# Kernel tuning notes

Measured on AMD Instinct MI355X. Metric: run time of the kernel, lower is better.

Reference implementation:

```python
import jax, jax.numpy as jnp
import numpy as np

B, L, D, H = 4, 1024, 1024, 16
HD = D // H
SCALE = 1.0 / np.sqrt(HD)
NOISE_PROB = 0.05
NOISE_SCALE = 0.1


def _linear(x, w, b):
    # torch nn.Linear convention: y = x @ W^T + b, W: [out, in]
    return x @ w.T + b


def _quantum_noise(key, real, imag, p=NOISE_PROB, s=NOISE_SCALE):
    """Phase flips, amplitude noise, and measurement dropout on a complex
    tensor represented as (real, imag). Deterministic given `key`."""
    k_phase, k_amp, k_nr, k_ni, k_meas = jax.random.split(key, 5)
    shape = real.shape
    flip = jnp.where(jax.random.uniform(k_phase, shape) < p, -1.0, 1.0)
    amp_mask = (jax.random.uniform(k_amp, shape) < p).astype(real.dtype)
    new_r = real * flip + jax.random.normal(k_nr, shape, real.dtype) * s * amp_mask
    new_i = imag * flip + jax.random.normal(k_ni, shape, imag.dtype) * s * amp_mask
    keep = 1.0 - (jax.random.uniform(k_meas, shape) < p * 0.5).astype(real.dtype)
    return new_r * keep, new_i * keep


def _heads(t):
    # [B, L, D] -> [B, H, L, HD]
    b, l, _ = t.shape
    return t.reshape(b, l, H, HD).transpose(0, 2, 1, 3)


def setup_inputs() -> dict:
    key = jax.random.key(0)
    ks = jax.random.split(key, 16)
    inp = {
        "x_real": jax.random.normal(ks[0], (B, L, D), jnp.float32),
        "x_imag": jax.random.normal(ks[1], (B, L, D), jnp.float32),
        "mask": jnp.ones((B, L), jnp.int32),
    }
    names = ["qr", "qi", "kr", "ki", "vr", "vi", "or", "oi"]
    for i, n in enumerate(names):
        inp[n + "_w"] = jax.random.normal(ks[2 + i], (D, D), jnp.float32) * 0.02
        inp[n + "_b"] = jnp.zeros((D,), jnp.float32)
    ent = jnp.eye(H) + (jax.random.normal(ks[10], (H, H)) * 0.1) * (
        jax.random.uniform(ks[11], (H, H)) < 0.2
    ).astype(jnp.float32)
    inp["ent"] = ent
    return inp


def reference(x_real, x_imag, mask, qr_w, qr_b, qi_w, qi_b, kr_w, kr_b,
              ki_w, ki_b, vr_w, vr_b, vi_w, vi_b, or_w, or_b, oi_w, oi_b, ent):
    # complex Q/K/V: real part from x.real, imag part from x.imag
    q_r, q_i = _linear(x_real, qr_w, qr_b), _linear(x_imag, qi_w, qi_b)
    k_r, k_i = _linear(x_real, kr_w, kr_b), _linear(x_imag, ki_w, ki_b)
    v_r, v_i = _linear(x_real, vr_w, vr_b), _linear(x_imag, vi_w, vi_b)

    nkey = jax.random.key(1)
    q_r, q_i = _quantum_noise(jax.random.fold_in(nkey, 0), q_r, q_i)
    k_r, k_i = _quantum_noise(jax.random.fold_in(nkey, 1), k_r, k_i)
    v_r, v_i = _quantum_noise(jax.random.fold_in(nkey, 2), v_r, v_i)

    q_r, q_i, k_r, k_i, v_r, v_i = map(_heads, (q_r, q_i, k_r, k_i, v_r, v_i))

    # torch.einsum('bhld,hh->bhld') == per-head scaling by diag(ent)
    d = jnp.diagonal(ent)[None, :, None, None]
    q_r, q_i = q_r * d, q_i * d
    k_r, k_i = k_r * d, k_i * d

    # Re(q . conj(k)) interference score: [B, H, Lq, Lk]
    scores = (jnp.einsum("bhqd,bhkd->bhqk", q_r, k_r)
              + jnp.einsum("bhqd,bhkd->bhqk", q_i, k_i)) * SCALE
    scores = jnp.where(mask[:, None, None, :] == 0, -1e9, scores)
    attn = jax.nn.softmax(scores, axis=-1)

    out_r = jnp.einsum("bhqk,bhkd->bhqd", attn, v_r)
    out_i = jnp.einsum("bhqk,bhkd->bhqd", attn, v_i)
    out_r = out_r.transpose(0, 2, 1, 3).reshape(x_real.shape)
    out_i = out_i.transpose(0, 2, 1, 3).reshape(x_real.shape)

    out_real = _linear(out_r, or_w, or_b)
    out_imag = _linear(out_i, oi_w, oi_b)
    return out_real, out_imag, attn
```

## Files before the change

kernel.cpp:

```cpp
#include <hip/hip_runtime.h>
#include <cstdint>

#define PARTITIONABLE 1

static constexpr int Bsz = 4, Lsz = 1024, Dsz = 1024, Hn = 16, HDsz = 64;
static constexpr size_t ELEMS = (size_t)Bsz * Lsz * Dsz;
static constexpr uint32_t HALF_N = (uint32_t)(ELEMS / 2);
static constexpr float SCALE = 0.125f;
static constexpr float P_NOISE = 0.05f;
static constexpr float S_NOISE = 0.1f;
static constexpr size_t MBy = 1024 * 1024;

typedef unsigned short u16;
typedef uint64_t u64;
typedef __attribute__((ext_vector_type(8))) short short8v;
typedef __attribute__((ext_vector_type(4))) float floatx4;
typedef __attribute__((ext_vector_type(4))) unsigned int uint4v;

__device__ __forceinline__ void gload16(const u16* g, u16* l) {
  __builtin_amdgcn_global_load_lds(
      (const __attribute__((address_space(1))) void*)(g),
      (__attribute__((address_space(3))) void*)(l), 16, 0, 0);
}

__host__ __device__ __forceinline__ void tf2x32(uint32_t k0, uint32_t k1,
                                                uint32_t x0, uint32_t x1,
                                                uint32_t& o0, uint32_t& o1) {
  uint32_t ks2 = k0 ^ k1 ^ 0x1BD11BDAu;
  x0 += k0; x1 += k1;
#define TFR(r) { x0 += x1; x1 = (x1 << (r)) | (x1 >> (32 - (r))); x1 ^= x0; }
  TFR(13) TFR(15) TFR(26) TFR(6)
  x0 += k1; x1 += ks2 + 1u;
  TFR(17) TFR(29) TFR(16) TFR(24)
  x0 += ks2; x1 += k0 + 2u;
  TFR(13) TFR(15) TFR(26) TFR(6)
  x0 += k0; x1 += k1 + 3u;
  TFR(17) TFR(29) TFR(16) TFR(24)
  x0 += k1; x1 += ks2 + 4u;
  TFR(13) TFR(15) TFR(26) TFR(6)
  x0 += ks2; x1 += k0 + 5u;
#undef TFR
  o0 = x0; o1 = x1;
}

struct KeySet { uint32_t k[5][2]; };
struct AllKeys { KeySet t[3]; };

__device__ __forceinline__ uint32_t draw_bits(uint32_t k0, uint32_t k1, uint32_t idx) {
#if PARTITIONABLE
  uint32_t o0, o1; tf2x32(k0, k1, 0u, idx, o0, o1);
  return o0 ^ o1;
#else
  uint32_t o0, o1;
  if (idx < HALF_N) { tf2x32(k0, k1, idx, idx + HALF_N, o0, o1); return o0; }
  tf2x32(k0, k1, idx - HALF_N, idx, o0, o1); return o1;
#endif
}

__device__ __forceinline__ float unif01(uint32_t bits) {
  return __uint_as_float((bits >> 9) | 0x3f800000u) - 1.0f;
}

__device__ __forceinline__ float normal_from_bits(uint32_t bits) {
  const float LO = -0.99999994f;
  float f = unif01(bits);
  float x = fmaxf(LO, f * 2.0f + LO);
  float w = -log1pf(-x * x);
  float p;
  if (w < 5.0f) {
    w = w - 2.5f;
    p = 2.81022636e-08f;
    p = fmaf(p, w, 3.43273939e-07f);
    p = fmaf(p, w, -3.5233877e-06f);
    p = fmaf(p, w, -4.39150654e-06f);
    p = fmaf(p, w, 0.00021858087f);
    p = fmaf(p, w, -0.00125372503f);
    p = fmaf(p, w, -0.00417768164f);
    p = fmaf(p, w, 0.246640727f);
    p = fmaf(p, w, 1.50140941f);
  } else {
    w = sqrtf(w) - 3.0f;
    p = -0.000200214257f;
    p = fmaf(p, w, 0.000100950558f);
    p = fmaf(p, w, 0.00134934322f);
    p = fmaf(p, w, -0.00367342844f);
    p = fmaf(p, w, 0.00573950773f);
    p = fmaf(p, w, -0.0076224613f);
    p = fmaf(p, w, 0.00943887047f);
    p = fmaf(p, w, 1.00167406f);
    p = fmaf(p, w, 2.83297682f);
  }
  return 1.41421356f * (p * x);
}

__device__ __forceinline__ uint32_t bf16_rn(float f) {
  uint32_t u = __float_as_uint(f);
  return (u + 0x7FFFu + ((u >> 16) & 1u)) >> 16;
}
__device__ __forceinline__ float bf2f(uint32_t h) { return __uint_as_float(h << 16); }
__device__ __forceinline__ void cvt_split(float4 v, u64& hi, u64& lo) {
  uint32_t h0 = bf16_rn(v.x), h1 = bf16_rn(v.y), h2 = bf16_rn(v.z), h3 = bf16_rn(v.w);
  float r0 = v.x - bf2f(h0), r1 = v.y - bf2f(h1), r2 = v.z - bf2f(h2), r3 = v.w - bf2f(h3);
  uint32_t l0 = bf16_rn(r0), l1 = bf16_rn(r1), l2 = bf16_rn(r2), l3 = bf16_rn(r3);
  hi = (u64)h0 | ((u64)h1 << 16) | ((u64)h2 << 32) | ((u64)h3 << 48);
  lo = (u64)l0 | ((u64)l1 << 16) | ((u64)l2 << 32) | ((u64)l3 << 48);
}

__device__ __forceinline__ void mfma_tile(const u16* Ahs, const u16* Als,
                                          const u16* Bhs, const u16* Bls,
                                          int l, int wm, int wn, floatx4 acc[4][4]) {
#pragma unroll
  for (int c = 0; c < 2; ++c) {
    const int pr = (l ^ (l >> 4) ^ (c << 2)) & 63;
    short8v aH[4], aL[4], bH[4], bL[4];
#pragma unroll
    for (int t = 0; t < 4; ++t) {
      const int ia = ((c * 8 + wm * 4 + t) * 64 + pr) * 8;
      aH[t] = *(const short8v*)&Ahs[ia]; aL[t] = *(const short8v*)&Als[ia];
      const int ib = ((c * 8 + wn * 4 + t) * 64 + pr) * 8;
      bH[t] = *(const short8v*)&Bhs[ib]; bL[t] = *(const short8v*)&Bls[ib];
    }
#pragma unroll
    for (int mt = 0; mt < 4; ++mt)
#pragma unroll
      for (int nt = 0; nt < 4; ++nt) {
        acc[mt][nt] = __builtin_amdgcn_mfma_f32_16x16x32_bf16(aH[mt], bH[nt], acc[mt][nt], 0, 0, 0);
        acc[mt][nt] = __builtin_amdgcn_mfma_f32_16x16x32_bf16(aH[mt], bL[nt], acc[mt][nt], 0, 0, 0);
        acc[mt][nt] = __builtin_amdgcn_mfma_f32_16x16x32_bf16(aL[mt], bH[nt], acc[mt][nt], 0, 0, 0);
      }
  }
}

__device__ __forceinline__ void mfma_step(const u16* Ahs, const u16* Als,
                                          const u16* Bhs, const u16* Bls,
                                          int pr, int wm, int wn, floatx4 acc[4][4]) {
  short8v aH[4], aL[4], bH[4], bL[4];
#pragma unroll
  for (int t = 0; t < 4; ++t) {
    const int ia = ((wm * 4 + t) * 64 + pr) * 8;
    aH[t] = *(const short8v*)&Ahs[ia]; aL[t] = *(const short8v*)&Als[ia];
    const int ib = ((wn * 4 + t) * 64 + pr) * 8;
    bH[t] = *(const short8v*)&Bhs[ib]; bL[t] = *(const short8v*)&Bls[ib];
  }
#pragma unroll
  for (int mt = 0; mt < 4; ++mt)
#pragma unroll
    for (int nt = 0; nt < 4; ++nt) {
      acc[mt][nt] = __builtin_amdgcn_mfma_f32_16x16x32_bf16(aH[mt], bH[nt], acc[mt][nt], 0, 0, 0);
      acc[mt][nt] = __builtin_amdgcn_mfma_f32_16x16x32_bf16(aH[mt], bL[nt], acc[mt][nt], 0, 0, 0);
      acc[mt][nt] = __builtin_amdgcn_mfma_f32_16x16x32_bf16(aL[mt], bH[nt], acc[mt][nt], 0, 0, 0);
    }
}

struct SJob { const float* src; u16* dh; u16* dl; int n4; };
struct SJobs { SJob j[8]; };

__global__ __launch_bounds__(256) void split8_kernel(SJobs js) {
  const SJob J = js.j[blockIdx.y];
  int i = blockIdx.x * 256 + (int)threadIdx.x;
  if (i >= J.n4) return;
  float4 v = ((const float4*)J.src)[i];
  u64 h, l; cvt_split(v, h, l);
  ((u64*)J.dh)[i] = h; ((u64*)J.dl)[i] = l;
}

struct GJob { const u16* Ah; const u16* Al; const u16* Wh; const u16* Wl;
              const float* bias; float* Yf; u16* Yh; u16* Yl; };
struct GJobs { GJob j[6]; };

template<int MODE>
__global__ __launch_bounds__(256, 2) void gemm_kernel(GJobs jobs) {
  const GJob J = jobs.j[blockIdx.z];
  const int n0 = blockIdx.x * 128, m0 = blockIdx.y * 128;
  __shared__ u16 Ahs[8192], Als[8192], Bhs[8192], Bls[8192];
  const int tid = (int)threadIdx.x, w = tid >> 6, l = tid & 63;
  const int wm = w >> 1, wn = w & 1;
  const int cA = w >> 1, m2A = l >> 4;
  const int qA = (l ^ m2A ^ (cA << 2)) & 15;
  const int colA = cA * 32 + m2A * 8;
  const int tb = (w & 1) * 4;

  const u16* ahp = J.Ah + (size_t)(m0 + qA) * Dsz + colA;
  const u16* alp = J.Al + (size_t)(m0 + qA) * Dsz + colA;
  const u16* whp = J.Wh + (size_t)(n0 + qA) * Dsz + colA;
  const u16* wlp = J.Wl + (size_t)(n0 + qA) * Dsz + colA;

  floatx4 acc[4][4];
#pragma unroll
  for (int i = 0; i < 4; ++i)
#pragma unroll
    for (int j = 0; j < 4; ++j) acc[i][j] = (floatx4){0.f, 0.f, 0.f, 0.f};

  for (int k0 = 0; k0 < Dsz; k0 += 64) {
    __syncthreads();
#pragma unroll
    for (int i = 0; i < 4; ++i) {
      const size_t go = (size_t)((tb + i) * 16) * Dsz + k0;
      gload16(ahp + go, &Ahs[(w * 4 + i) * 512]);
      gload16(alp + go, &Als[(w * 4 + i) * 512]);
      gload16(whp + go, &Bhs[(w * 4 + i) * 512]);
      gload16(wlp + go, &Bls[(w * 4 + i) * 512]);
    }
    __syncthreads();
    mfma_tile(Ahs, Als, Bhs, Bls, l, wm, wn, acc);
  }

  const int colLane = l & 15, rquad = l >> 4;
#pragma unroll
  for (int nt = 0; nt < 4; ++nt) {
    const int col = n0 + wn * 64 + nt * 16 + colLane;
    const float bv = J.bias[col];
#pragma unroll
    for (int mt = 0; mt < 4; ++mt) {
      const int r0 = m0 + wm * 64 + mt * 16 + rquad * 4;
#pragma unroll
      for (int j2 = 0; j2 < 4; ++j2) {
        float v = acc[mt][nt][j2] + bv;
        if (MODE == 1) {
          J.Yf[(size_t)(r0 + j2) * Dsz + col] = v;
        } else {
          const uint32_t hi = bf16_rn(v);
          const uint32_t lo = bf16_rn(v - bf2f(hi));
          J.Yh[(size_t)(r0 + j2) * Dsz + col] = (u16)hi;
          J.Yl[(size_t)(r0 + j2) * Dsz + col] = (u16)lo;
        }
      }
    }
  }
}

__global__ __launch_bounds__(256) void noise_kernel(
    u16* __restrict__ qhr, u16* __restrict__ qlr, u16* __restrict__ qhi, u16* __restrict__ qli,
    u16* __restrict__ khr, u16* __restrict__ klr, u16* __restrict__ khi, u16* __restrict__ kli,
    u16* __restrict__ vhr, u16* __restrict__ vlr, u16* __restrict__ vhi, u16* __restrict__ vli,
    const float* __restrict__ ent, AllKeys keys) {
  const uint32_t e = blockIdx.x * 256u + threadIdx.x;
  const int j = (int)blockIdx.y;
  u16 *rh, *rl, *ih, *il;
  if (j == 0) { rh = qhr; rl = qlr; ih = qhi; il = qli; }
  else if (j == 1) { rh = khr; rl = klr; ih = khi; il = kli; }
  else { rh = vhr; rl = vlr; ih = vhi; il = vli; }
  const KeySet& ks = keys.t[j];
  const uint32_t b_phase = draw_bits(ks.k[0][0], ks.k[0][1], e);
  const uint32_t b_amp   = draw_bits(ks.k[1][0], ks.k[1][1], e);
  const uint32_t b_nr    = draw_bits(ks.k[2][0], ks.k[2][1], e);
  const uint32_t b_ni    = draw_bits(ks.k[3][0], ks.k[3][1], e);
  const uint32_t b_meas  = draw_bits(ks.k[4][0], ks.k[4][1], e);
  const float flip = (unif01(b_phase) < P_NOISE) ? -1.0f : 1.0f;
  const float amp  = (unif01(b_amp)  < P_NOISE) ? 1.0f : 0.0f;
  const float keep = (unif01(b_meas) < P_NOISE * 0.5f) ? 0.0f : 1.0f;
  const float nr = normal_from_bits(b_nr);
  const float ni = normal_from_bits(b_ni);
  float r  = bf2f(rh[e]) + bf2f(rl[e]);
  float iv = bf2f(ih[e]) + bf2f(il[e]);
  r  = (r  * flip + nr * S_NOISE * amp) * keep;
  iv = (iv * flip + ni * S_NOISE * amp) * keep;
  if (j != 2) {
    const int h = ((int)e & (Dsz - 1)) >> 6;
    const float d = ent[h * Hn + h];
    r *= d; iv *= d;
  }
  uint32_t hr = bf16_rn(r);  rh[e] = (u16)hr; rl[e] = (u16)bf16_rn(r - bf2f(hr));
  uint32_t hi2 = bf16_rn(iv); ih[e] = (u16)hi2; il[e] = (u16)bf16_rn(iv - bf2f(hi2));
}

__global__ __launch_bounds__(256, 2) void scores_kernel(
    const u16* __restrict__ qhr, const u16* __restrict__ qlr,
    const u16* __restrict__ qhi, const u16* __restrict__ qli,
    const u16* __restrict__ khr, const u16* __restrict__ klr,
    const u16* __restrict__ khi, const u16* __restrict__ kli,
    const int* __restrict__ mask, float* __restrict__ attn) {
  const int bh = (int)blockIdx.z;
  const int b = bh >> 4, h = bh & 15;
  const int n0 = blockIdx.x * 128, m0 = blockIdx.y * 128;
  __shared__ u16 Ahs[2][4096], Als[2][4096], Bhs[2][4096], Bls[2][4096];
  const int tid = (int)threadIdx.x, w = tid >> 6, l = tid & 63;
  const int wm = w >> 1, wn = w & 1;
  const int qA = (l ^ (l >> 4)) & 15, colA = (l >> 4) * 8;
  const int pr = (l ^ (l >> 4)) & 63;
  const int t0 = w * 2, t1 = w * 2 + 1;

  const size_t aoff = ((size_t)(b * Lsz) + m0 + qA) * Dsz + h * HDsz + colA;
  const size_t boff = ((size_t)(b * Lsz) + n0 + qA) * Dsz + h * HDsz + colA;

  floatx4 acc[4][4];
#pragma unroll
  for (int i = 0; i < 4; ++i)
#pragma unroll
    for (int j = 0; j < 4; ++j) acc[i][j] = (floatx4){0.f, 0.f, 0.f, 0.f};

#define STGS(bufi, AH, AL, BH, BL, K0V) { \
    const size_t g0 = (size_t)(t0 * 16) * Dsz + (K0V); \
    const size_t g1 = (size_t)(t1 * 16) * Dsz + (K0V); \
    gload16(AH + aoff + g0, &Ahs[bufi][t0 * 512]); gload16(AH + aoff + g1, &Ahs[bufi][t1 * 512]); \
    gload16(AL + aoff + g0, &Als[bufi][t0 * 512]); gload16(AL + aoff + g1, &Als[bufi][t1 * 512]); \
    gload16(BH + boff + g0, &Bhs[bufi][t0 * 512]); gload16(BH + boff + g1, &Bhs[bufi][t1 * 512]); \
    gload16(BL + boff + g0, &Bls[bufi][t0 * 512]); gload16(BL + boff + g1, &Bls[bufi][t1 * 512]); }

  STGS(0, qhr, qlr, khr, klr, 0)
  __syncthreads();
  STGS(1, qhr, qlr, khr, klr, 32)
  mfma_step(Ahs[0], Als[0], Bhs[0], Bls[0], pr, wm, wn, acc);
  __syncthreads();
  STGS(0, qhi, qli, khi, kli, 0)
  mfma_step(Ahs[1], Als[1], Bhs[1], Bls[1], pr, wm, wn, acc);
  __syncthreads();
  STGS(1, qhi, qli, khi, kli, 32)
  mfma_step(Ahs[0], Als[0], Bhs[0], Bls[0], pr, wm, wn, acc);
  __syncthreads();
  mfma_step(Ahs[1], Als[1], Bhs[1], Bls[1], pr, wm, wn, acc);
#undef STGS

  const int colLane = l & 15, rquad = l >> 4;
#pragma unroll
  for (int nt = 0; nt < 4; ++nt) {
    const int col = n0 + wn * 64 + nt * 16 + colLane;
    const int mv = mask[b * Lsz + col];
#pragma unroll
    for (int mt = 0; mt < 4; ++mt) {
      const int r0 = m0 + wm * 64 + mt * 16 + rquad * 4;
#pragma unroll
      for (int j = 0; j < 4; ++j)
        attn[((size_t)bh * Lsz + r0 + j) * Lsz + col] =
            (mv == 0) ? -1e9f : acc[mt][nt][j] * SCALE;
    }
  }
}

__global__ __launch_bounds__(256) void vtrans_kernel(
    const u16* __restrict__ vhr, const u16* __restrict__ vlr,
    const u16* __restrict__ vhi, const u16* __restrict__ vli,
    u16* __restrict__ vth, u16* __restrict__ vtl) {
  const int bh = (int)blockIdx.y;
  const int b = bh >> 4, h = bh & 15;
  const int k0 = blockIdx.x * 64;
  __shared__ uint32_t T[128 * 65];
  const int t = (int)threadIdx.x;
  const int krow = t >> 4, d4 = (t & 15) * 4;

#pragma unroll
  for (int src = 0; src < 2; ++src) {
    const u16* VH = src ? vhi : vhr;
    const u16* VL = src ? vli : vlr;
    const int nb = src * 64;
#pragma unroll
    for (int p = 0; p < 4; ++p) {
      const int k = p * 16 + krow;
      const size_t off = ((size_t)(b * Lsz) + k0 + k) * Dsz + h * HDsz + d4;
      u64 hv = *(const u64*)(VH + off);
      u64 lv = *(const u64*)(VL + off);
#pragma unroll
      for (int e = 0; e < 4; ++e) {
        uint32_t hi = (uint32_t)((hv >> (16 * e)) & 0xFFFFu);
        uint32_t lo = (uint32_t)((lv >> (16 * e)) & 0xFFFFu);
        T[(nb + d4 + e) * 65 + k] = lo | (hi << 16);
      }
    }
  }
  __syncthreads();
  const int n = t >> 1, hf = t & 1;
  const size_t rowb = ((size_t)bh * 128 + n) * Lsz + k0 + hf * 32;
#pragma unroll
  for (int g = 0; g < 4; ++g) {
    uint32_t wv[8];
#pragma unroll
    for (int u = 0; u < 8; ++u) wv[u] = T[n * 65 + hf * 32 + g * 8 + u];
    uint4v hvv, lvv;
    hvv.x = (wv[0] >> 16) | (wv[1] & 0xFFFF0000u);
    hvv.y = (wv[2] >> 16) | (wv[3] & 0xFFFF0000u);
    hvv.z = (wv[4] >> 16) | (wv[5] & 0xFFFF0000u);
    hvv.w = (wv[6] >> 16) | (wv[7] & 0xFFFF0000u);
    lvv.x = (wv[0] & 0xFFFFu) | (wv[1] << 16);
    lvv.y = (wv[2] & 0xFFFFu) | (wv[3] << 16);
    lvv.z = (wv[4] & 0xFFFFu) | (wv[5] << 16);
    lvv.w = (wv[6] & 0xFFFFu) | (wv[7] << 16);
    *(uint4v*)&vth[rowb + g * 8] = hvv;
    *(uint4v*)&vtl[rowb + g * 8] = lvv;
  }
}

__global__ __launch_bounds__(256) void rowstat_kernel(const float* __restrict__ S,
                                                      float* __restrict__ rowm,
                                                      float* __restrict__ rowsum) {
  const int wv = (int)threadIdx.x >> 6, lane = (int)threadIdx.x & 63;
  const size_t row = (size_t)blockIdx.x * 4 + wv;
  const float* p = S + row * Lsz;
  float4 v[4];
#pragma unroll
  for (int i = 0; i < 4; ++i) v[i] = *(const float4*)(p + i * 256 + lane * 4);
  float m = -3.402823466e38f;
#pragma unroll
  for (int i = 0; i < 4; ++i)
    m = fmaxf(m, fmaxf(fmaxf(v[i].x, v[i].y), fmaxf(v[i].z, v[i].w)));
#pragma unroll
  for (int d = 1; d < 64; d <<= 1) m = fmaxf(m, __shfl_xor(m, d));
  float s = 0.f;
#pragma unroll
  for (int i = 0; i < 4; ++i)
    s += expf(v[i].x - m) + expf(v[i].y - m) + expf(v[i].z - m) + expf(v[i].w - m);
#pragma unroll
  for (int d = 1; d < 64; d <<= 1) s += __shfl_xor(s, d);
  if (lane == 0) { rowm[row] = m; rowsum[row] = s; }
}

__global__ __launch_bounds__(256, 2) void pv_kernel(
    float* __restrict__ attn, const u16* __restrict__ vth, const u16* __restrict__ vtl,
    const float* __restrict__ rowm, const float* __restrict__ rowsum,
    u16* __restrict__ ohr, u16* __restrict__ olr,
    u16* __restrict__ ohi, u16* __restrict__ oli) {
  const int bh = (int)blockIdx.y;
  const int b = bh >> 4, h = bh & 15;
  const int m0 = blockIdx.x * 128;
  __shared__ u16 Ahs[2][4096], Als[2][4096], Bhs[2][4096], Bls[2][4096];
  const int tid = (int)threadIdx.x, w = tid >> 6, l = tid & 63;
  const int wm = w >> 1, wn = w & 1;
  const int qA = (l ^ (l >> 4)) & 15, colA = (l >> 4) * 8;
  const int pr = (l ^ (l >> 4)) & 63;
  const int t0 = w * 2, t1 = w * 2 + 1;

  const int ar = tid >> 3, akq = tid & 7;
  const int am2 = akq >> 1, ahalf = akq & 1;
  int aidx[4];
  float rmv[4], inv[4];
#pragma unroll
  for (int rr = 0; rr < 4; ++rr) {
    const int trow = ar + rr * 32;
    const int p = ((trow & 15) + 16 * am2) ^ am2;
    aidx[rr] = ((trow >> 4) * 64 + p) * 8 + ahalf * 4;
    const size_t grow = (size_t)bh * Lsz + m0 + trow;
    rmv[rr] = rowm[grow]; inv[rr] = 1.0f / rowsum[grow];
  }
  float* arp = attn + ((size_t)bh * Lsz + m0 + ar) * Lsz + akq * 4;
  const u16* bhp = vth + ((size_t)bh * 128 + qA) * Lsz + colA;
  const u16* blp = vtl + ((size_t)bh * 128 + qA) * Lsz + colA;

  floatx4 acc[4][4];
#pragma unroll
  for (int i = 0; i < 4; ++i)
#pragma unroll
    for (int j = 0; j < 4; ++j) acc[i][j] = (floatx4){0.f, 0.f, 0.f, 0.f};

#define STGB(bufi, K0V) { \
    const size_t g0 = (size_t)(t0 * 16) * Lsz + (K0V); \
    const size_t g1 = (size_t)(t1 * 16) * Lsz + (K0V); \
    gload16(bhp + g0, &Bhs[bufi][t0 * 512]); gload16(bhp + g1, &Bhs[bufi][t1 * 512]); \
    gload16(blp + g0, &Bls[bufi][t0 * 512]); gload16(blp + g1, &Bls[bufi][t1 * 512]); }

#define LOADA(K0V, A4) { \
    _Pragma("unroll") for (int rr = 0; rr < 4; ++rr) \
      A4[rr] = *(const float4*)(arp + (size_t)(rr * 32) * Lsz + (K0V)); }

#define PROCA(bufi, K0V, A4) { \
    _Pragma("unroll") for (int rr = 0; rr < 4; ++rr) { \
      float4 p4; \
      p4.x = expf(A4[rr].x - rmv[rr]) * inv[rr]; \
      p4.y = expf(A4[rr].y - rmv[rr]) * inv[rr]; \
      p4.z = expf(A4[rr].z - rmv[rr]) * inv[rr]; \
      p4.w = expf(A4[rr].w - rmv[rr]) * inv[rr]; \
      *(float4*)(arp + (size_t)(rr * 32) * Lsz + (K0V)) = p4; \
      u64 h64, l64; cvt_split(p4, h64, l64); \
      *(u64*)&Ahs[bufi][aidx[rr]] = h64; *(u64*)&Als[bufi][aidx[rr]] = l64; } }

  {
    float4 a4[4];
    LOADA(0, a4)
    STGB(0, 0)
    PROCA(0, 0, a4)
  }
  __syncthreads();
  for (int kt = 0; kt < 32; kt += 2) {
    float4 n4[4];
    if (kt + 1 < 32) { LOADA((size_t)(kt + 1) * 32, n4) STGB(1, (size_t)(kt + 1) * 32) }
    mfma_step(Ahs[0], Als[0], Bhs[0], Bls[0], pr, wm, wn, acc);
    if (kt + 1 < 32) PROCA(1, (size_t)(kt + 1) * 32, n4)
    __syncthreads();
    if (kt + 2 < 32) { LOADA((size_t)(kt + 2) * 32, n4) STGB(0, (size_t)(kt + 2) * 32) }
    mfma_step(Ahs[1], Als[1], Bhs[1], Bls[1], pr, wm, wn, acc);
    if (kt + 2 < 32) PROCA(0, (size_t)(kt + 2) * 32, n4)
    __syncthreads();
  }
#undef STGB
#undef LOADA
#undef PROCA

  const int colLane = l & 15, rquad = l >> 4;
#pragma unroll
  for (int nt = 0; nt < 4; ++nt) {
    const int col = wn * 64 + nt * 16 + colLane;
    u16* oh = (col < 64) ? ohr : ohi;
    u16* ol = (col < 64) ? olr : oli;
    const int dcol = col & 63;
#pragma unroll
    for (int mt = 0; mt < 4; ++mt) {
      const int r0 = m0 + wm * 64 + mt * 16 + rquad * 4;
#pragma unroll
      for (int j = 0; j < 4; ++j) {
        float v = acc[mt][nt][j];
        const uint32_t hi = bf16_rn(v);
        const uint32_t lo = bf16_rn(v - bf2f(hi));
        const size_t oidx = ((size_t)(b * Lsz) + r0 + j) * Dsz + h * HDsz + dcol;
        oh[oidx] = (u16)hi; ol[oidx] = (u16)lo;
      }
    }
  }
}

extern "C" void kernel_launch(void* const* d_in, const int* in_sizes, int n_in,
                              void* d_out, int out_size, void* d_ws, size_t ws_size,
                              hipStream_t stream) {
  const float* x_real = (const float*)d_in[0];
  const float* x_imag = (const float*)d_in[1];
  const int*   mask   = (const int*)d_in[2];
  const float* pw[6] = {(const float*)d_in[3], (const float*)d_in[5], (const float*)d_in[7],
                        (const float*)d_in[9], (const float*)d_in[11], (const float*)d_in[13]};
  const float* pb[6] = {(const float*)d_in[4], (const float*)d_in[6], (const float*)d_in[8],
                        (const float*)d_in[10], (const float*)d_in[12], (const float*)d_in[14]};
  const float* or_w = (const float*)d_in[15]; const float* or_b = (const float*)d_in[16];
  const float* oi_w = (const float*)d_in[17]; const float* oi_b = (const float*)d_in[18];
  const float* ent  = (const float*)d_in[19];

  float* out_real = (float*)d_out;
  float* out_imag = out_real + ELEMS;
  float* attn     = out_imag + ELEMS;

  if (ws_size < 96 * MBy) return;
  uint8_t* wsb = (uint8_t*)d_ws;
  u16* qhr = (u16*)(wsb + 0 * MBy);  u16* qlr = (u16*)(wsb + 8 * MBy);
  u16* qhi = (u16*)(wsb + 16 * MBy); u16* qli = (u16*)(wsb + 24 * MBy);
  u16* khr = (u16*)(wsb + 32 * MBy); u16* klr = (u16*)(wsb + 40 * MBy);
  u16* khi = (u16*)(wsb + 48 * MBy); u16* kli = (u16*)(wsb + 56 * MBy);
  u16* xhr = (u16*)(wsb + 64 * MBy); u16* xlr = (u16*)(wsb + 72 * MBy);
  u16* xhi = (u16*)(wsb + 80 * MBy); u16* xli = (u16*)(wsb + 88 * MBy);
  u16* vth = (u16*)(wsb + 64 * MBy); u16* vtl = (u16*)(wsb + 80 * MBy);
  u16* ohr = (u16*)(wsb + 0 * MBy);  u16* olr = (u16*)(wsb + 8 * MBy);
  u16* ohi = (u16*)(wsb + 16 * MBy); u16* oli = (u16*)(wsb + 24 * MBy);
  u16* owh[2] = {(u16*)(wsb + 32 * MBy), (u16*)(wsb + 36 * MBy)};
  u16* owl[2] = {(u16*)(wsb + 34 * MBy), (u16*)(wsb + 38 * MBy)};

  uint8_t* atb = (uint8_t*)attn;
  u16* vhr = (u16*)(atb + 0 * MBy);  u16* vlr = (u16*)(atb + 8 * MBy);
  u16* vhi = (u16*)(atb + 16 * MBy); u16* vli = (u16*)(atb + 24 * MBy);

  float* rowm = out_real;
  float* rowsum = out_real + 65536;

  AllKeys keys;
  for (int j = 0; j < 3; ++j) {
    uint32_t a, b2;
    tf2x32(0u, 1u, 0u, (uint32_t)j, a, b2);
#if PARTITIONABLE
    for (int i = 0; i < 5; ++i)
      tf2x32(a, b2, 0u, (uint32_t)i, keys.t[j].k[i][0], keys.t[j].k[i][1]);
#else
    uint32_t out10[10];
    for (int i = 0; i < 5; ++i) {
      uint32_t o0, o1; tf2x32(a, b2, (uint32_t)i, (uint32_t)(i + 5), o0, o1);
      out10[i] = o0; out10[i + 5] = o1;
    }
    for (int i = 0; i < 5; ++i) { keys.t[j].k[i][0] = out10[2*i]; keys.t[j].k[i][1] = out10[2*i+1]; }
#endif
  }

  u16* pwh[6]; u16* pwl[6];
  for (int z = 0; z < 6; ++z) {
    pwh[z] = (u16*)(atb + 32 * MBy + (size_t)z * 4 * MBy);
    pwl[z] = pwh[z] + (size_t)Dsz * Dsz;
  }
  SJobs sj{};
  sj.j[0] = {x_real, xhr, xlr, (int)(ELEMS / 4)};
  sj.j[1] = {x_imag, xhi, xli, (int)(ELEMS / 4)};
  for (int z = 0; z < 6; ++z) sj.j[2 + z] = {pw[z], pwh[z], pwl[z], Dsz * Dsz / 4};
  split8_kernel<<<dim3(4096, 8), 256, 0, stream>>>(sj);

  GJobs pj{};
  u16* yh[6] = {qhr, qhi, khr, khi, vhr, vhi};
  u16* yl[6] = {qlr, qli, klr, kli, vlr, vli};
  const u16* ah6[6] = {xhr, xhi, xhr, xhi, xhr, xhi};
  const u16* al6[6] = {xlr, xli, xlr, xli, xlr, xli};
  for (int z = 0; z < 6; ++z) {
    pj.j[z].Ah = ah6[z]; pj.j[z].Al = al6[z];
    pj.j[z].Wh = pwh[z]; pj.j[z].Wl = pwl[z];
    pj.j[z].bias = pb[z]; pj.j[z].Yf = nullptr; pj.j[z].Yh = yh[z]; pj.j[z].Yl = yl[z];
  }
  gemm_kernel<0><<<dim3(8, 32, 6), 256, 0, stream>>>(pj);

  noise_kernel<<<dim3((uint32_t)(ELEMS / 256), 3), 256, 0, stream>>>(
      qhr, qlr, qhi, qli, khr, klr, khi, kli, vhr, vlr, vhi, vli, ent, keys);

  vtrans_kernel<<<dim3(16, 64), 256, 0, stream>>>(vhr, vlr, vhi, vli, vth, vtl);

  scores_kernel<<<dim3(8, 8, 64), 256, 0, stream>>>(
      qhr, qlr, qhi, qli, khr, klr, khi, kli, mask, attn);

  SJobs so{};
  so.j[0] = {or_w, owh[0], owl[0], Dsz * Dsz / 4};
  so.j[1] = {oi_w, owh[1], owl[1], Dsz * Dsz / 4};
  split8_kernel<<<dim3(1024, 2), 256, 0, stream>>>(so);

  rowstat_kernel<<<dim3(16384), 256, 0, stream>>>(attn, rowm, rowsum);

  pv_kernel<<<dim3(8, 64), 256, 0, stream>>>(attn, vth, vtl, rowm, rowsum,
                                             ohr, olr, ohi, oli);

  GJobs oj{};
  oj.j[0].Ah = ohr; oj.j[0].Al = olr; oj.j[0].Wh = owh[0]; oj.j[0].Wl = owl[0];
  oj.j[0].bias = or_b; oj.j[0].Yf = out_real;
  oj.j[1].Ah = ohi; oj.j[1].Al = oli; oj.j[1].Wh = owh[1]; oj.j[1].Wl = owl[1];
  oj.j[1].bias = oi_b; oj.j[1].Yf = out_imag;
  gemm_kernel<1><<<dim3(8, 32, 2), 256, 0, stream>>>(oj);
}
```

Measured before the change: 821.4 us.

## Fuse softmax row statistics into scores epilogue and double-buffer projection GEMM

The scores kernel now computes per-tile row max and sum-of-exponentials in its epilogue, reducing them across lanes and warps into per-block partials. A small rowstat2 kernel merges the 8 partials per row, replacing a pass that re-read the full 256MB score matrix. Separately, the projection GEMM is restructured to double-buffer LDS with 32-wide K steps so global-to-LDS loads overlap MFMA work. The cost is extra epilogue exp and shuffle work in the scores kernel plus a partials scratch buffer placed inside out_real.

```diff
diff --git a/kernel.cpp b/kernel.cpp
--- a/kernel.cpp
+++ b/kernel.cpp
@@ -106,31 +106,6 @@
   lo = (u64)l0 | ((u64)l1 << 16) | ((u64)l2 << 32) | ((u64)l3 << 48);
 }
 
-__device__ __forceinline__ void mfma_tile(const u16* Ahs, const u16* Als,
-                                          const u16* Bhs, const u16* Bls,
-                                          int l, int wm, int wn, floatx4 acc[4][4]) {
-#pragma unroll
-  for (int c = 0; c < 2; ++c) {
-    const int pr = (l ^ (l >> 4) ^ (c << 2)) & 63;
-    short8v aH[4], aL[4], bH[4], bL[4];
-#pragma unroll
-    for (int t = 0; t < 4; ++t) {
-      const int ia = ((c * 8 + wm * 4 + t) * 64 + pr) * 8;
-      aH[t] = *(const short8v*)&Ahs[ia]; aL[t] = *(const short8v*)&Als[ia];
-      const int ib = ((c * 8 + wn * 4 + t) * 64 + pr) * 8;
-      bH[t] = *(const short8v*)&Bhs[ib]; bL[t] = *(const short8v*)&Bls[ib];
-    }
-#pragma unroll
-    for (int mt = 0; mt < 4; ++mt)
-#pragma unroll
-      for (int nt = 0; nt < 4; ++nt) {
-        acc[mt][nt] = __builtin_amdgcn_mfma_f32_16x16x32_bf16(aH[mt], bH[nt], acc[mt][nt], 0, 0, 0);
-        acc[mt][nt] = __builtin_amdgcn_mfma_f32_16x16x32_bf16(aH[mt], bL[nt], acc[mt][nt], 0, 0, 0);
-        acc[mt][nt] = __builtin_amdgcn_mfma_f32_16x16x32_bf16(aL[mt], bH[nt], acc[mt][nt], 0, 0, 0);
-      }
-  }
-}
-
 __device__ __forceinline__ void mfma_step(const u16* Ahs, const u16* Als,
                                           const u16* Bhs, const u16* Bls,
                                           int pr, int wm, int wn, floatx4 acc[4][4]) {
@@ -172,13 +147,12 @@
 __global__ __launch_bounds__(256, 2) void gemm_kernel(GJobs jobs) {
   const GJob J = jobs.j[blockIdx.z];
   const int n0 = blockIdx.x * 128, m0 = blockIdx.y * 128;
-  __shared__ u16 Ahs[8192], Als[8192], Bhs[8192], Bls[8192];
+  __shared__ u16 Ahs[2][4096], Als[2][4096], Bhs[2][4096], Bls[2][4096];
   const int tid = (int)threadIdx.x, w = tid >> 6, l = tid & 63;
   const int wm = w >> 1, wn = w & 1;
-  const int cA = w >> 1, m2A = l >> 4;
-  const int qA = (l ^ m2A ^ (cA << 2)) & 15;
-  const int colA = cA * 32 + m2A * 8;
-  const int tb = (w & 1) * 4;
+  const int qA = (l ^ (l >> 4)) & 15, colA = (l >> 4) * 8;
+  const int pr = (l ^ (l >> 4)) & 63;
+  const int t0 = w * 2, t1 = w * 2 + 1;
 
   const u16* ahp = J.Ah + (size_t)(m0 + qA) * Dsz + colA;
   const u16* alp = J.Al + (size_t)(m0 + qA) * Dsz + colA;
@@ -191,19 +165,25 @@
 #pragma unroll
     for (int j = 0; j < 4; ++j) acc[i][j] = (floatx4){0.f, 0.f, 0.f, 0.f};
 
-  for (int k0 = 0; k0 < Dsz; k0 += 64) {
+#define STG(bufi, K0V) { \
+    const size_t g0 = (size_t)(t0 * 16) * Dsz + (K0V); \
+    const size_t g1 = (size_t)(t1 * 16) * Dsz + (K0V); \
+    gload16(ahp + g0, &Ahs[bufi][t0 * 512]); gload16(ahp + g1, &Ahs[bufi][t1 * 512]); \
+    gload16(alp + g0, &Als[bufi][t0 * 512]); gload16(alp + g1, &Als[bufi][t1 * 512]); \
+    gload16(whp + g0, &Bhs[bufi][t0 * 512]); gload16(whp + g1, &Bhs[bufi][t1 * 512]); \
+    gload16(wlp + g0, &Bls[bufi][t0 * 512]); gload16(wlp + g1, &Bls[bufi][t1 * 512]); }
+
+  STG(0, 0)
+  __syncthreads();
+  for (int kt = 0; kt < 32; kt += 2) {
+    if (kt + 1 < 32) STG(1, (size_t)(kt + 1) * 32)
+    mfma_step(Ahs[0], Als[0], Bhs[0], Bls[0], pr, wm, wn, acc);
     __syncthreads();
-#pragma unroll
-    for (int i = 0; i < 4; ++i) {
-      const size_t go = (size_t)((tb + i) * 16) * Dsz + k0;
-      gload16(ahp + go, &Ahs[(w * 4 + i) * 512]);
-      gload16(alp + go, &Als[(w * 4 + i) * 512]);
-      gload16(whp + go, &Bhs[(w * 4 + i) * 512]);
-      gload16(wlp + go, &Bls[(w * 4 + i) * 512]);
-    }
+    if (kt + 2 < 32) STG(0, (size_t)(kt + 2) * 32)
+    mfma_step(Ahs[1], Als[1], Bhs[1], Bls[1], pr, wm, wn, acc);
     __syncthreads();
-    mfma_tile(Ahs, Als, Bhs, Bls, l, wm, wn, acc);
-  }
+  }
+#undef STG
 
   const int colLane = l & 15, rquad = l >> 4;
 #pragma unroll
@@ -269,11 +249,13 @@
     const u16* __restrict__ qhi, const u16* __restrict__ qli,
     const u16* __restrict__ khr, const u16* __restrict__ klr,
     const u16* __restrict__ khi, const u16* __restrict__ kli,
-    const int* __restrict__ mask, float* __restrict__ attn) {
+    const int* __restrict__ mask, float* __restrict__ attn,
+    float2* __restrict__ part) {
   const int bh = (int)blockIdx.z;
   const int b = bh >> 4, h = bh & 15;
   const int n0 = blockIdx.x * 128, m0 = blockIdx.y * 128;
   __shared__ u16 Ahs[2][4096], Als[2][4096], Bhs[2][4096], Bls[2][4096];
+  __shared__ float2 pstat[2][128];
   const int tid = (int)threadIdx.x, w = tid >> 6, l = tid & 63;
   const int wm = w >> 1, wn = w & 1;
   const int qA = (l ^ (l >> 4)) & 15, colA = (l >> 4) * 8;
@@ -312,19 +294,73 @@
 #undef STGS
 
   const int colLane = l & 15, rquad = l >> 4;
-#pragma unroll
-  for (int nt = 0; nt < 4; ++nt) {
-    const int col = n0 + wn * 64 + nt * 16 + colLane;
-    const int mv = mask[b * Lsz + col];
-#pragma unroll
-    for (int mt = 0; mt < 4; ++mt) {
-      const int r0 = m0 + wm * 64 + mt * 16 + rquad * 4;
+  int mv4[4];
+#pragma unroll
+  for (int nt = 0; nt < 4; ++nt)
+    mv4[nt] = mask[b * Lsz + n0 + wn * 64 + nt * 16 + colLane];
+
+  float sm[4][4], ss[4][4];
+#pragma unroll
+  for (int mt = 0; mt < 4; ++mt) {
+    const int r0 = m0 + wm * 64 + mt * 16 + rquad * 4;
+#pragma unroll
+    for (int j = 0; j < 4; ++j) {
+      float v4[4];
+#pragma unroll
+      for (int nt = 0; nt < 4; ++nt) {
+        const int col = n0 + wn * 64 + nt * 16 + colLane;
+        float v = (mv4[nt] == 0) ? -1e9f : acc[mt][nt][j] * SCALE;
+        attn[((size_t)bh * Lsz + r0 + j) * Lsz + col] = v;
+        v4[nt] = v;
+      }
+      float m4 = fmaxf(fmaxf(v4[0], v4[1]), fmaxf(v4[2], v4[3]));
+      float s4 = expf(v4[0] - m4) + expf(v4[1] - m4) + expf(v4[2] - m4) + expf(v4[3] - m4);
+      sm[mt][j] = m4; ss[mt][j] = s4;
+    }
+  }
+#pragma unroll
+  for (int d = 1; d < 16; d <<= 1) {
+#pragma unroll
+    for (int mt = 0; mt < 4; ++mt)
+#pragma unroll
+      for (int j = 0; j < 4; ++j) {
+        float om = __shfl_xor(sm[mt][j], d);
+        float os = __shfl_xor(ss[mt][j], d);
+        float mn = fmaxf(sm[mt][j], om);
+        ss[mt][j] = ss[mt][j] * expf(sm[mt][j] - mn) + os * expf(om - mn);
+        sm[mt][j] = mn;
+      }
+  }
+  if (colLane == 0) {
+#pragma unroll
+    for (int mt = 0; mt < 4; ++mt)
 #pragma unroll
       for (int j = 0; j < 4; ++j)
-        attn[((size_t)bh * Lsz + r0 + j) * Lsz + col] =
-            (mv == 0) ? -1e9f : acc[mt][nt][j] * SCALE;
-    }
-  }
+        pstat[wn][wm * 64 + mt * 16 + rquad * 4 + j] = make_float2(sm[mt][j], ss[mt][j]);
+  }
+  __syncthreads();
+  if (tid < 128) {
+    float2 a = pstat[0][tid], c = pstat[1][tid];
+    float mn = fmaxf(a.x, c.x);
+    float s = a.y * expf(a.x - mn) + c.y * expf(c.x - mn);
+    part[((size_t)bh * Lsz + m0 + tid) * 8 + blockIdx.x] = make_float2(mn, s);
+  }
+}
+
+__global__ __launch_bounds__(256) void rowstat2_kernel(const float2* __restrict__ part,
+                                                       float* __restrict__ rowm,
+                                                       float* __restrict__ rowsum) {
+  const size_t row = (size_t)blockIdx.x * 256 + threadIdx.x;
+  float2 p[8];
+#pragma unroll
+  for (int i = 0; i < 8; ++i) p[i] = part[row * 8 + i];
+  float m = p[0].x;
+#pragma unroll
+  for (int i = 1; i < 8; ++i) m = fmaxf(m, p[i].x);
+  float s = 0.f;
+#pragma unroll
+  for (int i = 0; i < 8; ++i) s += p[i].y * expf(p[i].x - m);
+  rowm[row] = m; rowsum[row] = s;
 }
 
 __global__ __launch_bounds__(256) void vtrans_kernel(
@@ -377,30 +413,6 @@
     *(uint4v*)&vth[rowb + g * 8] = hvv;
     *(uint4v*)&vtl[rowb + g * 8] = lvv;
   }
-}
-
-__global__ __launch_bounds__(256) void rowstat_kernel(const float* __restrict__ S,
-                                                      float* __restrict__ rowm,
-                                                      float* __restrict__ rowsum) {
-  const int wv = (int)threadIdx.x >> 6, lane = (int)threadIdx.x & 63;
-  const size_t row = (size_t)blockIdx.x * 4 + wv;
-  const float* p = S + row * Lsz;
-  float4 v[4];
-#pragma unroll
-  for (int i = 0; i < 4; ++i) v[i] = *(const float4*)(p + i * 256 + lane * 4);
-  float m = -3.402823466e38f;
-#pragma unroll
-  for (int i = 0; i < 4; ++i)
-    m = fmaxf(m, fmaxf(fmaxf(v[i].x, v[i].y), fmaxf(v[i].z, v[i].w)));
-#pragma unroll
-  for (int d = 1; d < 64; d <<= 1) m = fmaxf(m, __shfl_xor(m, d));
-  float s = 0.f;
-#pragma unroll
-  for (int i = 0; i < 4; ++i)
-    s += expf(v[i].x - m) + expf(v[i].y - m) + expf(v[i].z - m) + expf(v[i].w - m);
-#pragma unroll
-  for (int d = 1; d < 64; d <<= 1) s += __shfl_xor(s, d);
-  if (lane == 0) { rowm[row] = m; rowsum[row] = s; }
 }
 
 __global__ __launch_bounds__(256, 2) void pv_kernel(
@@ -543,6 +555,7 @@
 
   float* rowm = out_real;
   float* rowsum = out_real + 65536;
+  float2* part = (float2*)(out_real + 131072);
 
   AllKeys keys;
   for (int j = 0; j < 3; ++j) {
@@ -590,14 +603,14 @@
   vtrans_kernel<<<dim3(16, 64), 256, 0, stream>>>(vhr, vlr, vhi, vli, vth, vtl);
 
   scores_kernel<<<dim3(8, 8, 64), 256, 0, stream>>>(
-      qhr, qlr, qhi, qli, khr, klr, khi, kli, mask, attn);
+      qhr, qlr, qhi, qli, khr, klr, khi, kli, mask, attn, part);
 
   SJobs so{};
   so.j[0] = {or_w, owh[0], owl[0], Dsz * Dsz / 4};
   so.j[1] = {oi_w, owh[1], owl[1], Dsz * Dsz / 4};
   split8_kernel<<<dim3(1024, 2), 256, 0, stream>>>(so);
 
-  rowstat_kernel<<<dim3(16384), 256, 0, stream>>>(attn, rowm, rowsum);
+  rowstat2_kernel<<<dim3(256), 256, 0, stream>>>(part, rowm, rowsum);
 
   pv_kernel<<<dim3(8, 64), 256, 0, stream>>>(attn, vth, vtl, rowm, rowsum,
                                              ohr, olr, ohi, oli);
```

Measured after the change: 854.9 us. 4.1% more time.

## Fuse Q/K/V projections sharing an input into one GEMM kernel

Applied to the files above, without the earlier changes.

The projection GEMM now computes Q, K and V for the same input (real or imag) in one block, loading each A tile once and reusing it across three weight matrices. K-step drops from 64 to 32 columns per tile, and each block holds 48 accumulator tiles. This cuts A-operand global and LDS traffic by a factor of three. In exchange the grid shrinks from 1536 to 512 blocks, and register pressure may rise enough to hurt occupancy or spill.

```diff
diff --git a/kernel.cpp b/kernel.cpp
--- a/kernel.cpp
+++ b/kernel.cpp
@@ -164,12 +164,105 @@
   ((u64*)J.dh)[i] = h; ((u64*)J.dl)[i] = l;
 }
 
+struct GJob3 { const u16* Ah; const u16* Al;
+               const u16* Wh[3]; const u16* Wl[3];
+               const float* bias[3]; u16* Yh[3]; u16* Yl[3]; };
+struct GJobs3 { GJob3 j[2]; };
+
+__global__ __launch_bounds__(256, 2) void gemm3_kernel(GJobs3 jobs) {
+  const GJob3 J = jobs.j[blockIdx.z];
+  const int n0 = blockIdx.x * 128, m0 = blockIdx.y * 128;
+  __shared__ u16 Ahs[4096], Als[4096];
+  __shared__ u16 Bhs[3][4096], Bls[3][4096];
+  const int tid = (int)threadIdx.x, w = tid >> 6, l = tid & 63;
+  const int wm = w >> 1, wn = w & 1;
+  const int qA = (l ^ (l >> 4)) & 15, colA = (l >> 4) * 8;
+  const int pr = (l ^ (l >> 4)) & 63;
+  const int t0 = w * 2, t1 = w * 2 + 1;
+
+  const u16* ahp = J.Ah + (size_t)(m0 + qA) * Dsz + colA;
+  const u16* alp = J.Al + (size_t)(m0 + qA) * Dsz + colA;
+  const u16* whp0 = J.Wh[0] + (size_t)(n0 + qA) * Dsz + colA;
+  const u16* wlp0 = J.Wl[0] + (size_t)(n0 + qA) * Dsz + colA;
+  const u16* whp1 = J.Wh[1] + (size_t)(n0 + qA) * Dsz + colA;
+  const u16* wlp1 = J.Wl[1] + (size_t)(n0 + qA) * Dsz + colA;
+  const u16* whp2 = J.Wh[2] + (size_t)(n0 + qA) * Dsz + colA;
+  const u16* wlp2 = J.Wl[2] + (size_t)(n0 + qA) * Dsz + colA;
+
+  floatx4 acc[3][4][4];
+#pragma unroll
+  for (int z = 0; z < 3; ++z)
+#pragma unroll
+    for (int i = 0; i < 4; ++i)
+#pragma unroll
+      for (int j = 0; j < 4; ++j) acc[z][i][j] = (floatx4){0.f, 0.f, 0.f, 0.f};
+
+  for (int kt = 0; kt < 32; ++kt) {
+    const size_t g0 = (size_t)(t0 * 16) * Dsz + (size_t)kt * 32;
+    const size_t g1 = (size_t)(t1 * 16) * Dsz + (size_t)kt * 32;
+    __syncthreads();
+    gload16(ahp + g0, &Ahs[t0 * 512]);  gload16(ahp + g1, &Ahs[t1 * 512]);
+    gload16(alp + g0, &Als[t0 * 512]);  gload16(alp + g1, &Als[t1 * 512]);
+    gload16(whp0 + g0, &Bhs[0][t0 * 512]); gload16(whp0 + g1, &Bhs[0][t1 * 512]);
+    gload16(wlp0 + g0, &Bls[0][t0 * 512]); gload16(wlp0 + g1, &Bls[0][t1 * 512]);
+    gload16(whp1 + g0, &Bhs[1][t0 * 512]); gload16(whp1 + g1, &Bhs[1][t1 * 512]);
+    gload16(wlp1 + g0, &Bls[1][t0 * 512]); gload16(wlp1 + g1, &Bls[1][t1 * 512]);
+    gload16(whp2 + g0, &Bhs[2][t0 * 512]); gload16(whp2 + g1, &Bhs[2][t1 * 512]);
+    gload16(wlp2 + g0, &Bls[2][t0 * 512]); gload16(wlp2 + g1, &Bls[2][t1 * 512]);
+    __syncthreads();
+
+    short8v aH[4], aL[4];
+#pragma unroll
+    for (int t = 0; t < 4; ++t) {
+      const int ia = ((wm * 4 + t) * 64 + pr) * 8;
+      aH[t] = *(const short8v*)&Ahs[ia]; aL[t] = *(const short8v*)&Als[ia];
+    }
+#pragma unroll
+    for (int z = 0; z < 3; ++z) {
+#pragma unroll
+      for (int nt = 0; nt < 4; ++nt) {
+        const int ib = ((wn * 4 + nt) * 64 + pr) * 8;
+        short8v bH = *(const short8v*)&Bhs[z][ib];
+        short8v bL = *(const short8v*)&Bls[z][ib];
+#pragma unroll
+        for (int mt = 0; mt < 4; ++mt) {
+          acc[z][mt][nt] = __builtin_amdgcn_mfma_f32_16x16x32_bf16(aH[mt], bH, acc[z][mt][nt], 0, 0, 0);
+          acc[z][mt][nt] = __builtin_amdgcn_mfma_f32_16x16x32_bf16(aH[mt], bL, acc[z][mt][nt], 0, 0, 0);
+          acc[z][mt][nt] = __builtin_amdgcn_mfma_f32_16x16x32_bf16(aL[mt], bH, acc[z][mt][nt], 0, 0, 0);
+        }
+      }
+    }
+  }
+
+  const int colLane = l & 15, rquad = l >> 4;
+#pragma unroll
+  for (int z = 0; z < 3; ++z) {
+    u16* Yh = J.Yh[z]; u16* Yl = J.Yl[z];
+#pragma unroll
+    for (int nt = 0; nt < 4; ++nt) {
+      const int col = n0 + wn * 64 + nt * 16 + colLane;
+      const float bv = J.bias[z][col];
+#pragma unroll
+      for (int mt = 0; mt < 4; ++mt) {
+        const int r0 = m0 + wm * 64 + mt * 16 + rquad * 4;
+#pragma unroll
+        for (int j2 = 0; j2 < 4; ++j2) {
+          float v = acc[z][mt][nt][j2] + bv;
+          const uint32_t hi = bf16_rn(v);
+          const uint32_t lo = bf16_rn(v - bf2f(hi));
+          Yh[(size_t)(r0 + j2) * Dsz + col] = (u16)hi;
+          Yl[(size_t)(r0 + j2) * Dsz + col] = (u16)lo;
+        }
+      }
+    }
+  }
+}
+
 struct GJob { const u16* Ah; const u16* Al; const u16* Wh; const u16* Wl;
-              const float* bias; float* Yf; u16* Yh; u16* Yl; };
-struct GJobs { GJob j[6]; };
-
-template<int MODE>
-__global__ __launch_bounds__(256, 2) void gemm_kernel(GJobs jobs) {
+              const float* bias; float* Yf; };
+struct GJobs { GJob j[2]; };
+
+__global__ __launch_bounds__(256, 2) void gemm_f32_kernel(GJobs jobs) {
   const GJob J = jobs.j[blockIdx.z];
   const int n0 = blockIdx.x * 128, m0 = blockIdx.y * 128;
   __shared__ u16 Ahs[8192], Als[8192], Bhs[8192], Bls[8192];
@@ -214,17 +307,8 @@
     for (int mt = 0; mt < 4; ++mt) {
       const int r0 = m0 + wm * 64 + mt * 16 + rquad * 4;
 #pragma unroll
-      for (int j2 = 0; j2 < 4; ++j2) {
-        float v = acc[mt][nt][j2] + bv;
-        if (MODE == 1) {
-          J.Yf[(size_t)(r0 + j2) * Dsz + col] = v;
-        } else {
-          const uint32_t hi = bf16_rn(v);
-          const uint32_t lo = bf16_rn(v - bf2f(hi));
-          J.Yh[(size_t)(r0 + j2) * Dsz + col] = (u16)hi;
-          J.Yl[(size_t)(r0 + j2) * Dsz + col] = (u16)lo;
-        }
-      }
+      for (int j2 = 0; j2 < 4; ++j2)
+        J.Yf[(size_t)(r0 + j2) * Dsz + col] = acc[mt][nt][j2] + bv;
     }
   }
 }
@@ -572,17 +656,22 @@
   for (int z = 0; z < 6; ++z) sj.j[2 + z] = {pw[z], pwh[z], pwl[z], Dsz * Dsz / 4};
   split8_kernel<<<dim3(4096, 8), 256, 0, stream>>>(sj);
 
-  GJobs pj{};
-  u16* yh[6] = {qhr, qhi, khr, khi, vhr, vhi};
-  u16* yl[6] = {qlr, qli, klr, kli, vlr, vli};
-  const u16* ah6[6] = {xhr, xhi, xhr, xhi, xhr, xhi};
-  const u16* al6[6] = {xlr, xli, xlr, xli, xlr, xli};
-  for (int z = 0; z < 6; ++z) {
-    pj.j[z].Ah = ah6[z]; pj.j[z].Al = al6[z];
-    pj.j[z].Wh = pwh[z]; pj.j[z].Wl = pwl[z];
-    pj.j[z].bias = pb[z]; pj.j[z].Yf = nullptr; pj.j[z].Yh = yh[z]; pj.j[z].Yl = yl[z];
-  }
-  gemm_kernel<0><<<dim3(8, 32, 6), 256, 0, stream>>>(pj);
+  GJobs3 pj{};
+  pj.j[0].Ah = xhr; pj.j[0].Al = xlr;
+  pj.j[0].Wh[0] = pwh[0]; pj.j[0].Wl[0] = pwl[0]; pj.j[0].bias[0] = pb[0];
+  pj.j[0].Yh[0] = qhr; pj.j[0].Yl[0] = qlr;
+  pj.j[0].Wh[1] = pwh[2]; pj.j[0].Wl[1] = pwl[2]; pj.j[0].bias[1] = pb[2];
+  pj.j[0].Yh[1] = khr; pj.j[0].Yl[1] = klr;
+  pj.j[0].Wh[2] = pwh[4]; pj.j[0].Wl[2] = pwl[4]; pj.j[0].bias[2] = pb[4];
+  pj.j[0].Yh[2] = vhr; pj.j[0].Yl[2] = vlr;
+  pj.j[1].Ah = xhi; pj.j[1].Al = xli;
+  pj.j[1].Wh[0] = pwh[1]; pj.j[1].Wl[0] = pwl[1]; pj.j[1].bias[0] = pb[1];
+  pj.j[1].Yh[0] = qhi; pj.j[1].Yl[0] = qli;
+  pj.j[1].Wh[1] = pwh[3]; pj.j[1].Wl[1] = pwl[3]; pj.j[1].bias[1] = pb[3];
+  pj.j[1].Yh[1] = khi; pj.j[1].Yl[1] = kli;
+  pj.j[1].Wh[2] = pwh[5]; pj.j[1].Wl[2] = pwl[5]; pj.j[1].bias[2] = pb[5];
+  pj.j[1].Yh[2] = vhi; pj.j[1].Yl[2] = vli;
+  gemm3_kernel<<<dim3(8, 32, 2), 256, 0, stream>>>(pj);
 
   noise_kernel<<<dim3((uint32_t)(ELEMS / 256), 3), 256, 0, stream>>>(
       qhr, qlr, qhi, qli, khr, klr, khi, kli, vhr, vlr, vhi, vli, ent, keys);
@@ -607,5 +696,5 @@
   oj.j[0].bias = or_b; oj.j[0].Yf = out_real;
   oj.j[1].Ah = ohi; oj.j[1].Al = oli; oj.j[1].Wh = owh[1]; oj.j[1].Wl = owl[1];
   oj.j[1].bias = oi_b; oj.j[1].Yf = out_imag;
-  gemm_kernel<1><<<dim3(8, 32, 2), 256, 0, stream>>>(oj);
-}
+  gemm_f32_kernel<<<dim3(8, 32, 2), 256, 0, stream>>>(oj);
+}
```

Result: faster. 771.6 us (-6.1%).
